# Kernel optimization log

Hardware: AMD Instinct MI355X
Metric: run time of the kernel (lower is better)

The kernel has to match this reference:

```python
import jax, jax.numpy as jnp
import numpy as np

OUTPUT_SIZE = 32


def setup_inputs() -> dict:
    key = jax.random.key(0)
    k1, k2, k3 = jax.random.split(key, 3)
    B, T, D, H, O = 256, 512, 1024, 2048, OUTPUT_SIZE
    return {
        "x": jax.random.normal(k1, (B, T, D), dtype=jnp.float32),
        "W1": jax.random.normal(k2, (D + O, H), dtype=jnp.float32) * 0.02,
        "b1": jnp.zeros((H,), dtype=jnp.float32),
        "W2": jax.random.normal(k3, (H, O), dtype=jnp.float32) * 0.02,
        "b2": jnp.zeros((O,), dtype=jnp.float32),
    }


def reference(x, W1, b1, W2, b2):
    # x: [B, T, D]; sequential greedy decoding with previous-prediction feedback.
    B = x.shape[0]
    O = W2.shape[1]

    def step(prev_pred, x_t):
        # prev_pred: [B] int32 (class 0 at t=0, matching torch zero-init preds)
        oh = jax.nn.one_hot(prev_pred, O, dtype=x_t.dtype)           # [B, O]
        inp = jnp.concatenate([x_t, oh], axis=-1)                    # [B, D+O]
        h = jnp.tanh(inp @ W1 + b1)                                  # [B, H]
        logit = h @ W2 + b2                                          # [B, O]
        pred = jnp.argmax(logit, axis=-1).astype(jnp.int32)          # [B]
        return pred, (logit, pred)

    init = jnp.zeros((B,), dtype=jnp.int32)
    _, (logits_t, preds_t) = jax.lax.scan(step, init, jnp.swapaxes(x, 0, 1))
    logits = jnp.swapaxes(logits_t, 0, 1)  # [B, T, O]
    preds = jnp.swapaxes(preds_t, 0, 1).astype(jnp.int64)  # [B, T]
    return logits, preds
```

## Files before the change

kernel.cpp:

```cpp
#include <hip/hip_runtime.h>
#include <cstdint>
#include <cstddef>

#define BATCH 256
#define SEQ   512
#define DIM   1024
#define HID   2048
#define NOUT  32

#define BM 256
#define BN 256
#define BK 64
#define KT_PER_SEG 16
#define KSTEPS 48
#define TM_TILES 512
#define TN_TILES 8
#define TILE_SHORTS (BM * BK)

typedef __attribute__((ext_vector_type(8))) short  short8;
typedef __attribute__((ext_vector_type(4))) float  f32x4;

__device__ __forceinline__ ushort f2bf(float v) {
    uint u = __builtin_bit_cast(uint, v);
    u = u + 0x7FFFu + ((u >> 16) & 1u);
    return (ushort)(u >> 16);
}
__device__ __forceinline__ float bf2f(ushort h) {
    uint u = ((uint)h) << 16;
    return __builtin_bit_cast(float, u);
}

__device__ __forceinline__ void gload16(const ushort* g, ushort* l) {
    __builtin_amdgcn_global_load_lds(
        (const __attribute__((address_space(1))) uint32_t*)(g),
        (__attribute__((address_space(3))) uint32_t*)(l),
        16, 0, 0);
}

__device__ __forceinline__ float fast_tanh(float x) {
    float e = __expf(2.0f * x);
    return 1.0f - 2.0f / (e + 1.0f);
}

__global__ __launch_bounds__(256) void prep_a(const float* __restrict__ x,
                                              ushort* __restrict__ Ah,
                                              ushort* __restrict__ Al)
{
    __shared__ alignas(16) ushort hi[TILE_SHORTS];
    __shared__ alignas(16) ushort lo[TILE_SHORTS];
    const int tm = blockIdx.x;
    const int kt = blockIdx.y;
    const int t  = threadIdx.x;

#pragma unroll
    for (int p = 0; p < 4; ++p) {
        const int row  = p * 64 + (t >> 2);
        const int part = t & 3;
        const float* src = x + (size_t)(tm * 256 + row) * DIM + kt * 64 + part * 16;
        float4 v0 = *(const float4*)(src);
        float4 v1 = *(const float4*)(src + 4);
        float4 v2 = *(const float4*)(src + 8);
        float4 v3 = *(const float4*)(src + 12);
        float av[16] = {v0.x, v0.y, v0.z, v0.w, v1.x, v1.y, v1.z, v1.w,
                        v2.x, v2.y, v2.z, v2.w, v3.x, v3.y, v3.z, v3.w};
#pragma unroll
        for (int g = 0; g < 2; ++g) {
            short8 hs, ls;
#pragma unroll
            for (int i = 0; i < 8; ++i) {
                float vv = av[g * 8 + i];
                ushort hh = f2bf(vv);
                hs[i] = (short)hh;
                ls[i] = (short)f2bf(vv - bf2f(hh));
            }
            const int kc = part * 2 + g;
            *(short8*)&hi[(kc * 256 + row) * 8] = hs;
            *(short8*)&lo[(kc * 256 + row) * 8] = ls;
        }
    }
    __syncthreads();
    const size_t tbase = ((size_t)tm * KT_PER_SEG + kt) * TILE_SHORTS;
#pragma unroll
    for (int i = 0; i < 8; ++i) {
        const int idx = i * 2048 + t * 8;
        *(short8*)(Ah + tbase + idx) = *(const short8*)(hi + idx);
        *(short8*)(Al + tbase + idx) = *(const short8*)(lo + idx);
    }
}

__global__ __launch_bounds__(256) void prep_b(const float* __restrict__ W1,
                                              ushort* __restrict__ Bh,
                                              ushort* __restrict__ Bl)
{
    __shared__ alignas(16) ushort hi[TILE_SHORTS];
    __shared__ alignas(16) ushort lo[TILE_SHORTS];
    const int tn = blockIdx.x;
    const int kt = blockIdx.y;
    const int t  = threadIdx.x;

#pragma unroll
    for (int p = 0; p < 16; ++p) {
        const int krow = p * 4 + (t >> 6);
        const int n4   = (t & 63) * 4;
        float4 v = *(const float4*)&W1[(size_t)(kt * 64 + krow) * HID + tn * 256 + n4];
        const int kc = krow >> 3, j = krow & 7;
        float vv[4] = {v.x, v.y, v.z, v.w};
#pragma unroll
        for (int q = 0; q < 4; ++q) {
            ushort hh = f2bf(vv[q]);
            hi[(kc * 256 + n4 + q) * 8 + j] = hh;
            lo[(kc * 256 + n4 + q) * 8 + j] = f2bf(vv[q] - bf2f(hh));
        }
    }
    __syncthreads();
    const size_t tbase = ((size_t)tn * KT_PER_SEG + kt) * TILE_SHORTS;
#pragma unroll
    for (int i = 0; i < 8; ++i) {
        const int idx = i * 2048 + t * 8;
        *(short8*)(Bh + tbase + idx) = *(const short8*)(hi + idx);
        *(short8*)(Bl + tbase + idx) = *(const short8*)(lo + idx);
    }
}

__global__ __launch_bounds__(512, 2) void gemm256(const ushort* __restrict__ Ah,
                                                  const ushort* __restrict__ Alo,
                                                  const ushort* __restrict__ Bh,
                                                  const ushort* __restrict__ Blo,
                                                  const float*  __restrict__ b1,
                                                  float* __restrict__ G)
{
    __shared__ alignas(16) ushort lds[2][2][TILE_SHORTS];

    const int tid  = threadIdx.x;
    const int lane = tid & 63;
    const int wave = tid >> 6;
    const int fr = lane & 15;
    const int fq = lane >> 4;
    const int wm = (wave >> 2) * 128;
    const int wn = (wave & 3) * 64;

    const int cpx = (TM_TILES * TN_TILES) >> 3;
    const int wg  = blockIdx.x;
    const int swz = (wg & 7) * cpx + (wg >> 3);
    const int tm  = swz >> 3;
    const int tn  = swz & 7;

    auto stage = [&](int buf, int ks) {
        const int seg = ks >> 4, kt = ks & 15;
        const ushort* at = ((seg == 2) ? Alo : Ah) + ((size_t)tm * KT_PER_SEG + kt) * TILE_SHORTS;
        const ushort* bt = ((seg == 1) ? Blo : Bh) + ((size_t)tn * KT_PER_SEG + kt) * TILE_SHORTS;
        ushort* la = &lds[buf][0][0];
        ushort* lb = &lds[buf][1][0];
#pragma unroll
        for (int i = 0; i < 4; ++i)
            gload16(at + i * 4096 + tid * 8, la + i * 4096 + tid * 8);
#pragma unroll
        for (int i = 0; i < 4; ++i)
            gload16(bt + i * 4096 + tid * 8, lb + i * 4096 + tid * 8);
    };

    f32x4 acc[8][4];
#pragma unroll
    for (int i = 0; i < 8; ++i)
#pragma unroll
        for (int j = 0; j < 4; ++j) {
            f32x4 z = {0.f, 0.f, 0.f, 0.f};
            acc[i][j] = z;
        }

    stage(0, 0);
    stage(1, 1);
    asm volatile("s_waitcnt vmcnt(8)" ::: "memory");
    __builtin_amdgcn_s_barrier();

    for (int ks = 0; ks < KSTEPS; ++ks) {
        const int cur = ks & 1;
        const ushort* LA = &lds[cur][0][0];
        const ushort* LB = &lds[cur][1][0];
#pragma unroll
        for (int kk = 0; kk < 2; ++kk) {
            const int kc = kk * 4 + fq;
            short8 a[8], b[4];
#pragma unroll
            for (int mt = 0; mt < 8; ++mt)
                a[mt] = *(const short8*)&LA[(kc * 256 + wm + mt * 16 + fr) * 8];
#pragma unroll
            for (int nt = 0; nt < 4; ++nt)
                b[nt] = *(const short8*)&LB[(kc * 256 + wn + nt * 16 + fr) * 8];
            __builtin_amdgcn_s_setprio(1);
#pragma unroll
            for (int mt = 0; mt < 8; ++mt)
#pragma unroll
                for (int nt = 0; nt < 4; ++nt)
                    acc[mt][nt] = __builtin_amdgcn_mfma_f32_16x16x32_bf16(a[mt], b[nt], acc[mt][nt], 0, 0, 0);
            __builtin_amdgcn_s_setprio(0);
        }
        asm volatile("" ::: "memory");
        __builtin_amdgcn_s_barrier();
        if (ks + 2 < KSTEPS) {
            stage(cur, ks + 2);
            asm volatile("s_waitcnt vmcnt(8)" ::: "memory");
        } else {
            asm volatile("s_waitcnt vmcnt(0)" ::: "memory");
        }
        __builtin_amdgcn_s_barrier();
    }

    const int m0 = tm * BM, n0 = tn * BN;
#pragma unroll
    for (int nt = 0; nt < 4; ++nt) {
        const int gn = n0 + wn + nt * 16 + fr;
        const float bias = b1[gn];
#pragma unroll
        for (int mt = 0; mt < 8; ++mt) {
            const int gm = m0 + wm + mt * 16 + fq * 4;
            float* out = G + (size_t)gm * HID + gn;
#pragma unroll
            for (int r = 0; r < 4; ++r)
                out[(size_t)r * HID] = acc[mt][nt][r] + bias;
        }
    }
}

__global__ __launch_bounds__(256) void split_w1t(const float* __restrict__ W1,
                                                 ushort* __restrict__ Bth,
                                                 ushort* __restrict__ Btl)
{
    __shared__ ushort th[32][33];
    __shared__ ushort tl[32][33];
    const int n0 = blockIdx.x * 32;
    const int k0 = blockIdx.y * 32;
    const int tx = threadIdx.x & 31;
    const int ty = threadIdx.x >> 5;
#pragma unroll
    for (int r = 0; r < 4; ++r) {
        int k = ty + r * 8;
        float v = W1[(size_t)(k0 + k) * HID + n0 + tx];
        ushort h = f2bf(v);
        th[k][tx] = h;
        tl[k][tx] = f2bf(v - bf2f(h));
    }
    __syncthreads();
#pragma unroll
    for (int r = 0; r < 4; ++r) {
        int n = ty + r * 8;
        Bth[(size_t)(n0 + n) * DIM + k0 + tx] = th[tx][n];
        Btl[(size_t)(n0 + n) * DIM + k0 + tx] = tl[tx][n];
    }
}

__global__ __launch_bounds__(256) void gemm_split(const float*  __restrict__ A,
                                                  const ushort* __restrict__ Bth,
                                                  const ushort* __restrict__ Btl,
                                                  const float*  __restrict__ b1,
                                                  float* __restrict__ G)
{
    __shared__ ushort Ahs[128][32];
    __shared__ ushort Als[128][32];
    __shared__ ushort Bhs[128][32];
    __shared__ ushort Bls[128][32];

    const int tid  = threadIdx.x;
    const int lane = tid & 63;
    const int wave = tid >> 6;
    const int n0 = blockIdx.x * 128;
    const int m0 = blockIdx.y * 128;
    const int wm = (wave & 1) * 64;
    const int wn = (wave >> 1) * 64;

    const int srow = tid >> 1;
    const int skc  = (tid & 1) * 16;
    const float*  aptr  = A   + (size_t)(m0 + srow) * DIM + skc;
    const ushort* bhptr = Bth + (size_t)(n0 + srow) * DIM + skc;
    const ushort* blptr = Btl + (size_t)(n0 + srow) * DIM + skc;

    const int fr = lane & 15;
    const int fq = lane >> 4;

    f32x4 acc[4][4];
#pragma unroll
    for (int i = 0; i < 4; ++i)
#pragma unroll
        for (int j = 0; j < 4; ++j) {
            f32x4 z = {0.f, 0.f, 0.f, 0.f};
            acc[i][j] = z;
        }

    for (int k0 = 0; k0 < DIM; k0 += 32) {
        float4 a0 = *(const float4*)(aptr + k0);
        float4 a1 = *(const float4*)(aptr + k0 + 4);
        float4 a2 = *(const float4*)(aptr + k0 + 8);
        float4 a3 = *(const float4*)(aptr + k0 + 12);
        short8 bh0 = *(const short8*)(bhptr + k0);
        short8 bh1 = *(const short8*)(bhptr + k0 + 8);
        short8 bl0 = *(const short8*)(blptr + k0);
        short8 bl1 = *(const short8*)(blptr + k0 + 8);

        __syncthreads();

        float av[16] = {a0.x, a0.y, a0.z, a0.w, a1.x, a1.y, a1.z, a1.w,
                        a2.x, a2.y, a2.z, a2.w, a3.x, a3.y, a3.z, a3.w};
        short8 h0, h1, l0, l1;
#pragma unroll
        for (int i = 0; i < 8; ++i) {
            ushort h = f2bf(av[i]);
            h0[i] = (short)h;
            l0[i] = (short)f2bf(av[i] - bf2f(h));
        }
#pragma unroll
        for (int i = 0; i < 8; ++i) {
            ushort h = f2bf(av[8 + i]);
            h1[i] = (short)h;
            l1[i] = (short)f2bf(av[8 + i] - bf2f(h));
        }
        *(short8*)&Ahs[srow][skc]     = h0;
        *(short8*)&Ahs[srow][skc + 8] = h1;
        *(short8*)&Als[srow][skc]     = l0;
        *(short8*)&Als[srow][skc + 8] = l1;
        *(short8*)&Bhs[srow][skc]     = bh0;
        *(short8*)&Bhs[srow][skc + 8] = bh1;
        *(short8*)&Bls[srow][skc]     = bl0;
        *(short8*)&Bls[srow][skc + 8] = bl1;

        __syncthreads();

        short8 afh[4], afl[4], bfh[4], bfl[4];
#pragma unroll
        for (int t = 0; t < 4; ++t) {
            afh[t] = *(const short8*)&Ahs[wm + t * 16 + fr][fq * 8];
            afl[t] = *(const short8*)&Als[wm + t * 16 + fr][fq * 8];
            bfh[t] = *(const short8*)&Bhs[wn + t * 16 + fr][fq * 8];
            bfl[t] = *(const short8*)&Bls[wn + t * 16 + fr][fq * 8];
        }
#pragma unroll
        for (int mt = 0; mt < 4; ++mt)
#pragma unroll
            for (int nt = 0; nt < 4; ++nt) {
                acc[mt][nt] = __builtin_amdgcn_mfma_f32_16x16x32_bf16(afh[mt], bfh[nt], acc[mt][nt], 0, 0, 0);
                acc[mt][nt] = __builtin_amdgcn_mfma_f32_16x16x32_bf16(afh[mt], bfl[nt], acc[mt][nt], 0, 0, 0);
                acc[mt][nt] = __builtin_amdgcn_mfma_f32_16x16x32_bf16(afl[mt], bfh[nt], acc[mt][nt], 0, 0, 0);
            }
    }

#pragma unroll
    for (int nt = 0; nt < 4; ++nt) {
        const int gn = n0 + wn + nt * 16 + fr;
        const float bias = b1[gn];
#pragma unroll
        for (int mt = 0; mt < 4; ++mt) {
            const int gmb = m0 + wm + mt * 16 + fq * 4;
            float* out = G + (size_t)gmb * HID + gn;
#pragma unroll
            for (int r = 0; r < 4; ++r)
                out[(size_t)r * HID] = acc[mt][nt][r] + bias;
        }
    }
}

__global__ __launch_bounds__(1024) void seq_scan(const float* __restrict__ G,
                                                 const float* __restrict__ W1,
                                                 const float* __restrict__ W2,
                                                 const float* __restrict__ b2,
                                                 float* __restrict__ out_logits,
                                                 float* __restrict__ out_preds)
{
    const int b   = blockIdx.x;
    const int t   = threadIdx.x;
    const int og  = t >> 8;
    const int j   = t & 255;
    const int o0  = og * 8;
    const int h0  = j * 8;

    __shared__ float hbuf[HID];
    __shared__ float partials[16][8];
    __shared__ int   pred_sh;

    float w2r[8][8];
#pragma unroll
    for (int i = 0; i < 8; ++i) {
        const float4* p4 = reinterpret_cast<const float4*>(&W2[(size_t)(h0 + i) * NOUT + o0]);
        float4 aa = p4[0], bbq = p4[1];
        w2r[i][0] = aa.x;  w2r[i][1] = aa.y;  w2r[i][2] = aa.z;  w2r[i][3] = aa.w;
        w2r[i][4] = bbq.x; w2r[i][5] = bbq.y; w2r[i][6] = bbq.z; w2r[i][7] = bbq.w;
    }

    int p = 0;
    const float* Gb = G + (size_t)b * SEQ * HID;
    float2 g = *reinterpret_cast<const float2*>(Gb + 2 * t);

    for (int step = 0; step < SEQ; ++step) {
        float2 u = *reinterpret_cast<const float2*>(&W1[(size_t)(DIM + p) * HID + 2 * t]);
        float hv0 = fast_tanh(g.x + u.x);
        float hv1 = fast_tanh(g.y + u.y);
        if (step + 1 < SEQ)
            g = *reinterpret_cast<const float2*>(Gb + (size_t)(step + 1) * HID + 2 * t);

        *reinterpret_cast<float2*>(&hbuf[2 * t]) = make_float2(hv0, hv1);
        __syncthreads();

        float4 ha = *reinterpret_cast<const float4*>(&hbuf[h0]);
        float4 hb = *reinterpret_cast<const float4*>(&hbuf[h0 + 4]);
        float hv[8] = {ha.x, ha.y, ha.z, ha.w, hb.x, hb.y, hb.z, hb.w};
        float acc[8];
#pragma unroll
        for (int c = 0; c < 8; ++c) acc[c] = 0.f;
#pragma unroll
        for (int i = 0; i < 8; ++i)
#pragma unroll
            for (int c = 0; c < 8; ++c)
                acc[c] = fmaf(hv[i], w2r[i][c], acc[c]);

#pragma unroll
        for (int off = 32; off; off >>= 1)
#pragma unroll
            for (int c = 0; c < 8; ++c)
                acc[c] += __shfl_xor(acc[c], off, 64);

        const int wave = t >> 6;
        const int lane = t & 63;
        if (lane == 0) {
#pragma unroll
            for (int c = 0; c < 8; ++c) partials[wave][c] = acc[c];
        }
        __syncthreads();

        if (t < 32) {
            const int o  = t;
            const int gq = o >> 3;
            const int c  = o & 7;
            float logit = b2[o] + partials[gq * 4 + 0][c] + partials[gq * 4 + 1][c]
                                + partials[gq * 4 + 2][c] + partials[gq * 4 + 3][c];
            out_logits[((size_t)b * SEQ + step) * NOUT + o] = logit;

            float v = logit; int idx = o;
#pragma unroll
            for (int off = 16; off; off >>= 1) {
                float ov = __shfl_xor(v, off, 32);
                int   oi = __shfl_xor(idx, off, 32);
                if (ov > v || (ov == v && oi < idx)) { v = ov; idx = oi; }
            }
            if (o == 0) {
                pred_sh = idx;
                out_preds[(size_t)b * SEQ + step] = (float)idx;
            }
        }
        __syncthreads();
        p = pred_sh;
    }
}

extern "C" void kernel_launch(void* const* d_in, const int* in_sizes, int n_in,
                              void* d_out, int out_size, void* d_ws, size_t ws_size,
                              hipStream_t stream) {
    const float* x  = (const float*)d_in[0];
    const float* W1 = (const float*)d_in[1];
    const float* b1 = (const float*)d_in[2];
    const float* W2 = (const float*)d_in[3];
    const float* b2 = (const float*)d_in[4];

    const size_t G_BYTES = (size_t)BATCH * SEQ * HID * sizeof(float);
    const size_t A_BYTES = (size_t)BATCH * SEQ * DIM * sizeof(ushort);
    const size_t B_BYTES = (size_t)HID * DIM * sizeof(ushort);

    float* G = (float*)d_ws;
    float* out_logits = (float*)d_out;
    float* out_preds  = (float*)d_out + (size_t)BATCH * SEQ * NOUT;

    const size_t need_new = G_BYTES + 2 * A_BYTES + 2 * B_BYTES;

    if (ws_size >= need_new) {
        ushort* Ah = (ushort*)((char*)d_ws + G_BYTES);
        ushort* Al = (ushort*)((char*)Ah + A_BYTES);
        ushort* Bh = (ushort*)((char*)Al + A_BYTES);
        ushort* Bl = (ushort*)((char*)Bh + B_BYTES);

        prep_a<<<dim3(TM_TILES, KT_PER_SEG), 256, 0, stream>>>(x, Ah, Al);
        prep_b<<<dim3(TN_TILES, KT_PER_SEG), 256, 0, stream>>>(W1, Bh, Bl);
        gemm256<<<dim3(TM_TILES * TN_TILES), 512, 0, stream>>>(Ah, Al, Bh, Bl, b1, G);
    } else {
        ushort* Bth = (ushort*)((char*)d_ws + G_BYTES);
        ushort* Btl = Bth + (size_t)HID * DIM;
        split_w1t<<<dim3(HID / 32, DIM / 32), 256, 0, stream>>>(W1, Bth, Btl);
        gemm_split<<<dim3(HID / 128, BATCH * SEQ / 128), 256, 0, stream>>>(x, Bth, Btl, b1, G);
    }

    seq_scan<<<BATCH, 1024, 0, stream>>>(G, W1, W2, b2, out_logits, out_preds);
}
```

Baseline: 4.177 ms.

## Split GEMM K-tile prefetch into halves and drop a barrier per scan step

```diff
diff --git a/kernel.cpp b/kernel.cpp
--- a/kernel.cpp
+++ b/kernel.cpp
@@ -145,18 +145,17 @@
     const int tm  = swz >> 3;
     const int tn  = swz & 7;
 
-    auto stage = [&](int buf, int ks) {
-        const int seg = ks >> 4, kt = ks & 15;
+    auto issue_half = [&](int s, int kk) {
+        const int seg = s >> 4, kt = s & 15;
         const ushort* at = ((seg == 2) ? Alo : Ah) + ((size_t)tm * KT_PER_SEG + kt) * TILE_SHORTS;
         const ushort* bt = ((seg == 1) ? Blo : Bh) + ((size_t)tn * KT_PER_SEG + kt) * TILE_SHORTS;
-        ushort* la = &lds[buf][0][0];
-        ushort* lb = &lds[buf][1][0];
-#pragma unroll
-        for (int i = 0; i < 4; ++i)
-            gload16(at + i * 4096 + tid * 8, la + i * 4096 + tid * 8);
-#pragma unroll
-        for (int i = 0; i < 4; ++i)
-            gload16(bt + i * 4096 + tid * 8, lb + i * 4096 + tid * 8);
+        ushort* la = &lds[s & 1][0][0];
+        ushort* lb = &lds[s & 1][1][0];
+        const int off0 = kk * 8192 + tid * 8;
+        gload16(at + off0,        la + off0);
+        gload16(at + off0 + 4096, la + off0 + 4096);
+        gload16(bt + off0,        lb + off0);
+        gload16(bt + off0 + 4096, lb + off0 + 4096);
     };
 
     f32x4 acc[8][4];
@@ -168,18 +167,17 @@
             acc[i][j] = z;
         }
 
-    stage(0, 0);
-    stage(1, 1);
-    asm volatile("s_waitcnt vmcnt(8)" ::: "memory");
-    __builtin_amdgcn_s_barrier();
-
-    for (int ks = 0; ks < KSTEPS; ++ks) {
-        const int cur = ks & 1;
-        const ushort* LA = &lds[cur][0][0];
-        const ushort* LB = &lds[cur][1][0];
-#pragma unroll
-        for (int kk = 0; kk < 2; ++kk) {
-            const int kc = kk * 4 + fq;
+    issue_half(0, 0);
+    issue_half(0, 1);
+
+    for (int s = 0; s < KSTEPS; ++s) {
+        const bool more = (s + 1 < KSTEPS);
+        asm volatile("s_waitcnt vmcnt(4)" ::: "memory");
+        asm volatile("s_barrier" ::: "memory");
+        {
+            const ushort* LA = &lds[s & 1][0][0];
+            const ushort* LB = &lds[s & 1][1][0];
+            const int kc = fq;
             short8 a[8], b[4];
 #pragma unroll
             for (int mt = 0; mt < 8; ++mt)
@@ -187,6 +185,7 @@
 #pragma unroll
             for (int nt = 0; nt < 4; ++nt)
                 b[nt] = *(const short8*)&LB[(kc * 256 + wn + nt * 16 + fr) * 8];
+            if (more) issue_half(s + 1, 0);
             __builtin_amdgcn_s_setprio(1);
 #pragma unroll
             for (int mt = 0; mt < 8; ++mt)
@@ -195,15 +194,29 @@
                     acc[mt][nt] = __builtin_amdgcn_mfma_f32_16x16x32_bf16(a[mt], b[nt], acc[mt][nt], 0, 0, 0);
             __builtin_amdgcn_s_setprio(0);
         }
-        asm volatile("" ::: "memory");
-        __builtin_amdgcn_s_barrier();
-        if (ks + 2 < KSTEPS) {
-            stage(cur, ks + 2);
-            asm volatile("s_waitcnt vmcnt(8)" ::: "memory");
-        } else {
-            asm volatile("s_waitcnt vmcnt(0)" ::: "memory");
-        }
-        __builtin_amdgcn_s_barrier();
+        if (more) { asm volatile("s_waitcnt vmcnt(4)" ::: "memory"); }
+        else      { asm volatile("s_waitcnt vmcnt(0)" ::: "memory"); }
+        asm volatile("s_barrier" ::: "memory");
+        {
+            const ushort* LA = &lds[s & 1][0][0];
+            const ushort* LB = &lds[s & 1][1][0];
+            const int kc = 4 + fq;
+            short8 a[8], b[4];
+#pragma unroll
+            for (int mt = 0; mt < 8; ++mt)
+                a[mt] = *(const short8*)&LA[(kc * 256 + wm + mt * 16 + fr) * 8];
+#pragma unroll
+            for (int nt = 0; nt < 4; ++nt)
+                b[nt] = *(const short8*)&LB[(kc * 256 + wn + nt * 16 + fr) * 8];
+            if (more) issue_half(s + 1, 1);
+            __builtin_amdgcn_s_setprio(1);
+#pragma unroll
+            for (int mt = 0; mt < 8; ++mt)
+#pragma unroll
+                for (int nt = 0; nt < 4; ++nt)
+                    acc[mt][nt] = __builtin_amdgcn_mfma_f32_16x16x32_bf16(a[mt], b[nt], acc[mt][nt], 0, 0, 0);
+            __builtin_amdgcn_s_setprio(0);
+        }
     }
 
     const int m0 = tm * BM, n0 = tn * BN;
@@ -370,10 +383,11 @@
     const int j   = t & 255;
     const int o0  = og * 8;
     const int h0  = j * 8;
+    const int lane = t & 63;
+    const int wv   = t >> 6;
 
     __shared__ float hbuf[HID];
     __shared__ float partials[16][8];
-    __shared__ int   pred_sh;
 
     float w2r[8][8];
 #pragma unroll
@@ -384,12 +398,16 @@
         w2r[i][4] = bbq.x; w2r[i][5] = bbq.y; w2r[i][6] = bbq.z; w2r[i][7] = bbq.w;
     }
 
+    const int  olane = lane & 31;
+    const float b2r  = b2[olane];
+
     int p = 0;
     const float* Gb = G + (size_t)b * SEQ * HID;
     float2 g = *reinterpret_cast<const float2*>(Gb + 2 * t);
 
     for (int step = 0; step < SEQ; ++step) {
-        float2 u = *reinterpret_cast<const float2*>(&W1[(size_t)(DIM + p) * HID + 2 * t]);
+        const int ps = __builtin_amdgcn_readfirstlane(p);
+        float2 u = *reinterpret_cast<const float2*>(&W1[(size_t)(DIM + ps) * HID + 2 * t]);
         float hv0 = fast_tanh(g.x + u.x);
         float hv1 = fast_tanh(g.y + u.y);
         if (step + 1 < SEQ)
@@ -416,36 +434,29 @@
             for (int c = 0; c < 8; ++c)
                 acc[c] += __shfl_xor(acc[c], off, 64);
 
-        const int wave = t >> 6;
-        const int lane = t & 63;
         if (lane == 0) {
 #pragma unroll
-            for (int c = 0; c < 8; ++c) partials[wave][c] = acc[c];
+            for (int c = 0; c < 8; ++c) partials[wv][c] = acc[c];
         }
         __syncthreads();
 
-        if (t < 32) {
-            const int o  = t;
-            const int gq = o >> 3;
-            const int c  = o & 7;
-            float logit = b2[o] + partials[gq * 4 + 0][c] + partials[gq * 4 + 1][c]
-                                + partials[gq * 4 + 2][c] + partials[gq * 4 + 3][c];
-            out_logits[((size_t)b * SEQ + step) * NOUT + o] = logit;
-
-            float v = logit; int idx = o;
-#pragma unroll
-            for (int off = 16; off; off >>= 1) {
-                float ov = __shfl_xor(v, off, 32);
-                int   oi = __shfl_xor(idx, off, 32);
-                if (ov > v || (ov == v && oi < idx)) { v = ov; idx = oi; }
-            }
-            if (o == 0) {
-                pred_sh = idx;
-                out_preds[(size_t)b * SEQ + step] = (float)idx;
-            }
-        }
-        __syncthreads();
-        p = pred_sh;
+        const int gq = olane >> 3;
+        const int c  = olane & 7;
+        float logit = b2r + partials[gq * 4 + 0][c] + partials[gq * 4 + 1][c]
+                          + partials[gq * 4 + 2][c] + partials[gq * 4 + 3][c];
+        if (t < 32)
+            out_logits[((size_t)b * SEQ + step) * NOUT + t] = logit;
+
+        float v = logit; int idx = olane;
+#pragma unroll
+        for (int off = 16; off; off >>= 1) {
+            float ov = __shfl_xor(v, off, 32);
+            int   oi = __shfl_xor(idx, off, 32);
+            if (ov > v || (ov == v && oi < idx)) { v = ov; idx = oi; }
+        }
+        if (t == 0)
+            out_preds[(size_t)b * SEQ + step] = (float)idx;
+        p = idx;
     }
 }
 
```

After: 4.243 ms. About the same (+1.6%).
